# Optimization experiments

Hardware: AMD Instinct MI355X
Metric: run time of the kernel (lower is better)

## Reference

```python
import jax, jax.numpy as jnp
import numpy as np
from jax import lax

# Stacked SimpleRNN (Keras): h_t = tanh(x_t @ W + h_{t-1} @ U + b).
# Dropout(0.5) is only active in training mode; this reference implements
# inference (training=None -> dropout disabled), matching model(x).

B, T, F = 512, 512, 78
HIDDENS = (16, 32, 64, 70)
NUM_CLASSES = 5


def _glorot(key, shape):
    fan_in, fan_out = shape[0], shape[1]
    lim = float(np.sqrt(6.0 / (fan_in + fan_out)))
    return jax.random.uniform(key, shape, jnp.float32, -lim, lim)


def setup_inputs() -> dict:
    key = jax.random.key(0)
    ks = jax.random.split(key, 16)
    x = jax.random.normal(ks[0], (B, T, F), jnp.float32)
    params = {}
    in_dim = F
    for i, h in enumerate(HIDDENS):
        params[f"W{i}"] = _glorot(ks[1 + 3 * i], (in_dim, h))
        params[f"U{i}"] = _glorot(ks[2 + 3 * i], (h, h))
        params[f"b{i}"] = jnp.zeros((h,), jnp.float32)
        in_dim = h
    params["Wd"] = _glorot(ks[13], (HIDDENS[-1], NUM_CLASSES))
    params["bd"] = jnp.zeros((NUM_CLASSES,), jnp.float32)
    return {"x": x, **params}


def _simple_rnn(x, W, U, b, return_sequences):
    # Precompute input projection for all timesteps: [B, T, H]
    xw = jnp.einsum("btf,fh->bth", x, W) + b
    h0 = jnp.zeros((x.shape[0], W.shape[1]), x.dtype)

    def step(h, xw_t):
        h_new = jnp.tanh(xw_t + h @ U)
        return h_new, h_new

    h_last, hs = lax.scan(step, h0, jnp.swapaxes(xw, 0, 1))  # scan over time
    if return_sequences:
        return jnp.swapaxes(hs, 0, 1)  # [B, T, H]
    return h_last  # [B, H]


def reference(x, W0, U0, b0, W1, U1, b1, W2, U2, b2, W3, U3, b3, Wd, bd):
    h = _simple_rnn(x, W0, U0, b0, True)
    h = _simple_rnn(h, W1, U1, b1, True)
    h = _simple_rnn(h, W2, U2, b2, True)
    h = _simple_rnn(h, W3, U3, b3, False)  # [B, 70]
    logits = h @ Wd + bd  # [B, 5]
    return jax.nn.softmax(logits, axis=-1)
```

## Files before the change

kernel.cpp:

```cpp
#include <hip/hip_runtime.h>
#include <cstddef>
#include <cstdint>


#define BB 512
#define TT 512
#define M_TOTAL (BB * TT)

__device__ __forceinline__ float tanh_fast(float x) {
  float ax = fabsf(x);
  float e = __expf(ax + ax);
  float r = 1.0f - 2.0f / (e + 1.0f);
  return (x >= 0.0f) ? r : -r;
}

__device__ __forceinline__ void fma4(float4& a, float s, const float4 w) {
  a.x = fmaf(s, w.x, a.x);
  a.y = fmaf(s, w.y, a.y);
  a.z = fmaf(s, w.z, a.z);
  a.w = fmaf(s, w.w, a.w);
}

template<int K, int N, int CG>
__global__ __launch_bounds__(256)
void proj_kernel(const float* __restrict__ in, const float* __restrict__ W,
                 const float* __restrict__ bias, float* __restrict__ out, int M)
{
  constexpr int NP = CG * 4;
  constexpr int RG = 256 / CG;
  __shared__ __align__(16) float wlds[K][NP];
  __shared__ __align__(16) float blds[NP];
  const int tid = threadIdx.x;
  for (int idx = tid; idx < K * NP; idx += 256) {
    int k = idx / NP, jj = idx - k * NP;
    wlds[k][jj] = (jj < N) ? W[k * N + jj] : 0.0f;
  }
  if (tid < NP) blds[tid] = (tid < N) ? bias[tid] : 0.0f;
  __syncthreads();

  const int c = tid % CG;
  const int rg = tid / CG;
  if (rg >= RG) return;
  const int j0 = c * 4;
  const long row0 = (long)blockIdx.x * (RG * 4) + (long)rg * 4;

  float4 b4 = *reinterpret_cast<const float4*>(&blds[j0]);
  float4 acc[4] = {b4, b4, b4, b4};
  const float* inp[4];
  bool rv[4];
  #pragma unroll
  for (int rr = 0; rr < 4; ++rr) {
    long rowi = row0 + rr;
    rv[rr] = rowi < M;
    inp[rr] = in + (rv[rr] ? rowi : 0) * (long)K;
  }

  int k = 0;
  for (; k + 4 <= K; k += 4) {
    float4 w0 = *reinterpret_cast<const float4*>(&wlds[k + 0][j0]);
    float4 w1 = *reinterpret_cast<const float4*>(&wlds[k + 1][j0]);
    float4 w2 = *reinterpret_cast<const float4*>(&wlds[k + 2][j0]);
    float4 w3 = *reinterpret_cast<const float4*>(&wlds[k + 3][j0]);
    #pragma unroll
    for (int rr = 0; rr < 4; ++rr) {
      float2 i0 = *reinterpret_cast<const float2*>(inp[rr] + k);
      float2 i1 = *reinterpret_cast<const float2*>(inp[rr] + k + 2);
      fma4(acc[rr], i0.x, w0);
      fma4(acc[rr], i0.y, w1);
      fma4(acc[rr], i1.x, w2);
      fma4(acc[rr], i1.y, w3);
    }
  }
  for (; k < K; ++k) {
    float4 w0 = *reinterpret_cast<const float4*>(&wlds[k][j0]);
    #pragma unroll
    for (int rr = 0; rr < 4; ++rr) fma4(acc[rr], inp[rr][k], w0);
  }

  #pragma unroll
  for (int rr = 0; rr < 4; ++rr) {
    if (!rv[rr]) continue;
    long obase = (row0 + rr) * (long)N + j0;
    if constexpr ((N % 4) == 0) {
      *reinterpret_cast<float4*>(&out[obase]) = acc[rr];
    } else {
      if (j0 + 4 <= N) {
        *reinterpret_cast<float2*>(&out[obase]) = make_float2(acc[rr].x, acc[rr].y);
        *reinterpret_cast<float2*>(&out[obase + 2]) = make_float2(acc[rr].z, acc[rr].w);
      } else {
        float v[4] = {acc[rr].x, acc[rr].y, acc[rr].z, acc[rr].w};
        #pragma unroll
        for (int jj = 0; jj < 4; ++jj)
          if (j0 + jj < N) out[obase + jj] = v[jj];
      }
    }
  }
}

template<int H, int ROWS, int BLK, bool LAST>
__global__ __launch_bounds__(BLK)
void rec_kernel(const float* __restrict__ xw, const float* __restrict__ U,
                float* __restrict__ hseq,
                const float* __restrict__ Wd, const float* __restrict__ bd,
                float* __restrict__ outp)
{
  constexpr int HP = (H + 3) & ~3;
  const int tid = threadIdx.x;
  const int r = tid / H;
  const int j = tid - r * H;
  const bool active = (r < ROWS);
  const int rc = active ? r : 0;
  int row = blockIdx.x * ROWS + r;
  if (row >= BB) row = BB - 1;

  __shared__ __align__(16) float hbuf[2][ROWS][HP];
  __shared__ float slog[8];
  for (int i = tid; i < 2 * ROWS * HP; i += BLK)
    reinterpret_cast<float*>(hbuf)[i] = 0.0f;

  float u[HP];
  #pragma unroll
  for (int kk = 0; kk < HP; ++kk)
    u[kk] = (kk < H && active) ? U[kk * H + j] : 0.0f;

  const float* xwrow = xw + ((size_t)row * TT) * H + j;
  float* hout = hseq + ((size_t)row * TT) * H + j;
  __syncthreads();

  float p0 = xwrow[0];
  float p1 = xwrow[H];
  for (int t = 0; t < TT; ++t) {
    float xv = p0;
    p0 = p1;
    int tn = (t + 2 < TT) ? (t + 2) : (TT - 1);
    p1 = xwrow[(size_t)tn * H];

    const float* hb = &hbuf[t & 1][rc][0];
    float a0 = xv, a1 = 0.0f, a2 = 0.0f, a3 = 0.0f;
    #pragma unroll
    for (int k4 = 0; k4 < HP / 4; ++k4) {
      float4 h4 = *reinterpret_cast<const float4*>(hb + 4 * k4);
      a0 = fmaf(h4.x, u[4 * k4 + 0], a0);
      a1 = fmaf(h4.y, u[4 * k4 + 1], a1);
      a2 = fmaf(h4.z, u[4 * k4 + 2], a2);
      a3 = fmaf(h4.w, u[4 * k4 + 3], a3);
    }
    float hn = tanh_fast((a0 + a1) + (a2 + a3));
    if (active) {
      hbuf[(t & 1) ^ 1][r][j] = hn;
      if constexpr (!LAST) hout[(size_t)t * H] = hn;
    }
    __syncthreads();
  }

  if constexpr (LAST) {
    if (tid < 5) {
      float l = bd[tid];
      #pragma unroll
      for (int kk = 0; kk < H; ++kk)
        l = fmaf(hbuf[0][0][kk], Wd[kk * 5 + tid], l);
      slog[tid] = l;
    }
    __syncthreads();
    if (tid < 5) {
      float m = slog[0];
      #pragma unroll
      for (int i = 1; i < 5; ++i) m = fmaxf(m, slog[i]);
      float s = 0.0f;
      #pragma unroll
      for (int i = 0; i < 5; ++i) s += __expf(slog[i] - m);
      outp[(size_t)blockIdx.x * 5 + tid] = __expf(slog[tid] - m) / s;
    }
  }
}

extern "C" void kernel_launch(void* const* d_in, const int* in_sizes, int n_in,
                              void* d_out, int out_size, void* d_ws, size_t ws_size,
                              hipStream_t stream)
{
  const float* x  = (const float*)d_in[0];
  const float* W0 = (const float*)d_in[1];
  const float* U0 = (const float*)d_in[2];
  const float* b0 = (const float*)d_in[3];
  const float* W1 = (const float*)d_in[4];
  const float* U1 = (const float*)d_in[5];
  const float* b1 = (const float*)d_in[6];
  const float* W2 = (const float*)d_in[7];
  const float* U2 = (const float*)d_in[8];
  const float* b2 = (const float*)d_in[9];
  const float* W3 = (const float*)d_in[10];
  const float* U3 = (const float*)d_in[11];
  const float* b3 = (const float*)d_in[12];
  const float* Wd = (const float*)d_in[13];
  const float* bd = (const float*)d_in[14];
  float* outp = (float*)d_out;

  float* A  = (float*)d_ws;
  float* Bv = (float*)((char*)d_ws + 73400320);

  const int M = M_TOTAL;

  proj_kernel<78, 16, 4><<<M / 256, 256, 0, stream>>>(x, W0, b0, A, M);
  rec_kernel<16, 4, 64, false><<<BB / 4, 64, 0, stream>>>(A, U0, Bv, Wd, bd, outp);
  proj_kernel<16, 32, 8><<<M / 128, 256, 0, stream>>>(Bv, W1, b1, A, M);
  rec_kernel<32, 2, 64, false><<<BB / 2, 64, 0, stream>>>(A, U1, Bv, Wd, bd, outp);
  proj_kernel<32, 64, 16><<<M / 64, 256, 0, stream>>>(Bv, W2, b2, A, M);
  rec_kernel<64, 1, 64, false><<<BB, 64, 0, stream>>>(A, U2, Bv, Wd, bd, outp);
  proj_kernel<64, 70, 18><<<(M + 55) / 56, 256, 0, stream>>>(Bv, W3, b3, A, M);
  rec_kernel<70, 1, 128, true><<<BB, 128, 0, stream>>>(A, U3, Bv, Wd, bd, outp);
}
```

Before: 1.129 ms.

## Run recurrence in a single wavefront without barriers and deeper prefetch

Every recurrent layer now runs in one 64-thread wavefront per block. The __syncthreads and double-buffered hidden state are replaced by a single LDS buffer, relying on lockstep wavefront execution. The H=70 layer gets its own kernel where the first six lanes compute two outputs each, so the block shrinks from 128 threads to one wave. The xw prefetch depth grows from 2 to 8 steps, and the final softmax uses wave shuffles. This removes per-step barrier cost but depends on implicit wave-synchronous LDS ordering, which may be fragile; register pressure also rises.

```diff
diff --git a/kernel.cpp b/kernel.cpp
--- a/kernel.cpp
+++ b/kernel.cpp
@@ -97,81 +97,136 @@
   }
 }
 
-template<int H, int ROWS, int BLK, bool LAST>
-__global__ __launch_bounds__(BLK)
+template<int H, int ROWS>
+__global__ __launch_bounds__(64, 1)
 void rec_kernel(const float* __restrict__ xw, const float* __restrict__ U,
-                float* __restrict__ hseq,
-                const float* __restrict__ Wd, const float* __restrict__ bd,
-                float* __restrict__ outp)
+                float* __restrict__ hseq)
 {
   constexpr int HP = (H + 3) & ~3;
+  constexpr int PF = 8;
   const int tid = threadIdx.x;
   const int r = tid / H;
   const int j = tid - r * H;
-  const bool active = (r < ROWS);
-  const int rc = active ? r : 0;
-  int row = blockIdx.x * ROWS + r;
-  if (row >= BB) row = BB - 1;
-
-  __shared__ __align__(16) float hbuf[2][ROWS][HP];
-  __shared__ float slog[8];
-  for (int i = tid; i < 2 * ROWS * HP; i += BLK)
-    reinterpret_cast<float*>(hbuf)[i] = 0.0f;
+  const int row = blockIdx.x * ROWS + r;
+
+  __shared__ __align__(16) float hlds[ROWS][HP];
+  for (int i = tid; i < ROWS * HP; i += 64)
+    reinterpret_cast<float*>(hlds)[i] = 0.0f;
+  __syncthreads();
 
   float u[HP];
   #pragma unroll
-  for (int kk = 0; kk < HP; ++kk)
-    u[kk] = (kk < H && active) ? U[kk * H + j] : 0.0f;
+  for (int kk = 0; kk < HP; ++kk) {
+    u[kk] = (kk < H) ? U[kk * H + j] : 0.0f;
+    asm volatile("" : "+v"(u[kk]));
+  }
 
   const float* xwrow = xw + ((size_t)row * TT) * H + j;
   float* hout = hseq + ((size_t)row * TT) * H + j;
+
+  float pf[PF];
+  #pragma unroll
+  for (int d = 0; d < PF; ++d) pf[d] = xwrow[(size_t)d * H];
+
+  for (int t = 0; t < TT; t += PF) {
+    #pragma unroll
+    for (int d = 0; d < PF; ++d) {
+      float xv = pf[d];
+      int tn = t + d + PF;
+      tn = (tn < TT) ? tn : (TT - 1);
+      pf[d] = xwrow[(size_t)tn * H];
+
+      const float* hb = &hlds[r][0];
+      float a0 = xv, a1 = 0.0f, a2 = 0.0f, a3 = 0.0f;
+      #pragma unroll
+      for (int k4 = 0; k4 < HP / 4; ++k4) {
+        float4 h4 = *reinterpret_cast<const float4*>(hb + 4 * k4);
+        a0 = fmaf(h4.x, u[4 * k4 + 0], a0);
+        a1 = fmaf(h4.y, u[4 * k4 + 1], a1);
+        a2 = fmaf(h4.z, u[4 * k4 + 2], a2);
+        a3 = fmaf(h4.w, u[4 * k4 + 3], a3);
+      }
+      float hn = tanh_fast((a0 + a1) + (a2 + a3));
+      hlds[r][j] = hn;
+      hout[(size_t)(t + d) * H] = hn;
+    }
+  }
+}
+
+__global__ __launch_bounds__(64, 1)
+void rec70_kernel(const float* __restrict__ xw, const float* __restrict__ U,
+                  const float* __restrict__ Wd, const float* __restrict__ bd,
+                  float* __restrict__ outp)
+{
+  constexpr int H = 70, HP = 72, PF = 8;
+  const int tid = threadIdx.x;
+  const int row = blockIdx.x;
+  const int j2 = (tid < 6) ? (64 + tid) : 69;
+
+  __shared__ __align__(16) float hlds[HP];
+  for (int i = tid; i < HP; i += 64) hlds[i] = 0.0f;
   __syncthreads();
 
-  float p0 = xwrow[0];
-  float p1 = xwrow[H];
-  for (int t = 0; t < TT; ++t) {
-    float xv = p0;
-    p0 = p1;
-    int tn = (t + 2 < TT) ? (t + 2) : (TT - 1);
-    p1 = xwrow[(size_t)tn * H];
-
-    const float* hb = &hbuf[t & 1][rc][0];
-    float a0 = xv, a1 = 0.0f, a2 = 0.0f, a3 = 0.0f;
-    #pragma unroll
-    for (int k4 = 0; k4 < HP / 4; ++k4) {
-      float4 h4 = *reinterpret_cast<const float4*>(hb + 4 * k4);
-      a0 = fmaf(h4.x, u[4 * k4 + 0], a0);
-      a1 = fmaf(h4.y, u[4 * k4 + 1], a1);
-      a2 = fmaf(h4.z, u[4 * k4 + 2], a2);
-      a3 = fmaf(h4.w, u[4 * k4 + 3], a3);
-    }
-    float hn = tanh_fast((a0 + a1) + (a2 + a3));
-    if (active) {
-      hbuf[(t & 1) ^ 1][r][j] = hn;
-      if constexpr (!LAST) hout[(size_t)t * H] = hn;
-    }
-    __syncthreads();
-  }
-
-  if constexpr (LAST) {
-    if (tid < 5) {
-      float l = bd[tid];
+  float u[HP], u2[HP];
+  #pragma unroll
+  for (int kk = 0; kk < HP; ++kk) {
+    u[kk]  = (kk < H) ? U[kk * H + tid] : 0.0f;
+    u2[kk] = (kk < H && tid < 6) ? U[kk * H + 64 + tid] : 0.0f;
+    asm volatile("" : "+v"(u[kk]), "+v"(u2[kk]));
+  }
+
+  const float* xwrow = xw + ((size_t)row * TT) * H;
+  float pfA[PF], pfB[PF];
+  #pragma unroll
+  for (int d = 0; d < PF; ++d) {
+    pfA[d] = xwrow[(size_t)d * H + tid];
+    pfB[d] = xwrow[(size_t)d * H + j2];
+  }
+
+  for (int t = 0; t < TT; t += PF) {
+    #pragma unroll
+    for (int d = 0; d < PF; ++d) {
+      float xvA = pfA[d], xvB = pfB[d];
+      int tn = t + d + PF;
+      tn = (tn < TT) ? tn : (TT - 1);
+      pfA[d] = xwrow[(size_t)tn * H + tid];
+      pfB[d] = xwrow[(size_t)tn * H + j2];
+
+      float a0 = xvA, a1 = 0.0f, a2 = 0.0f, a3 = 0.0f;
+      float b0 = xvB, b1 = 0.0f, b2 = 0.0f, b3 = 0.0f;
       #pragma unroll
-      for (int kk = 0; kk < H; ++kk)
-        l = fmaf(hbuf[0][0][kk], Wd[kk * 5 + tid], l);
-      slog[tid] = l;
-    }
-    __syncthreads();
-    if (tid < 5) {
-      float m = slog[0];
-      #pragma unroll
-      for (int i = 1; i < 5; ++i) m = fmaxf(m, slog[i]);
-      float s = 0.0f;
-      #pragma unroll
-      for (int i = 0; i < 5; ++i) s += __expf(slog[i] - m);
-      outp[(size_t)blockIdx.x * 5 + tid] = __expf(slog[tid] - m) / s;
-    }
-  }
+      for (int k4 = 0; k4 < HP / 4; ++k4) {
+        float4 h4 = *reinterpret_cast<const float4*>(&hlds[4 * k4]);
+        a0 = fmaf(h4.x, u[4 * k4 + 0], a0);
+        a1 = fmaf(h4.y, u[4 * k4 + 1], a1);
+        a2 = fmaf(h4.z, u[4 * k4 + 2], a2);
+        a3 = fmaf(h4.w, u[4 * k4 + 3], a3);
+        b0 = fmaf(h4.x, u2[4 * k4 + 0], b0);
+        b1 = fmaf(h4.y, u2[4 * k4 + 1], b1);
+        b2 = fmaf(h4.z, u2[4 * k4 + 2], b2);
+        b3 = fmaf(h4.w, u2[4 * k4 + 3], b3);
+      }
+      float hnA = tanh_fast((a0 + a1) + (a2 + a3));
+      float hnB = tanh_fast((b0 + b1) + (b2 + b3));
+      hlds[tid] = hnA;
+      if (tid < 6) hlds[64 + tid] = hnB;
+    }
+  }
+
+  float l = 0.0f;
+  if (tid < 5) {
+    l = bd[tid];
+    #pragma unroll
+    for (int kk = 0; kk < H; ++kk)
+      l = fmaf(hlds[kk], Wd[kk * 5 + tid], l);
+  }
+  float l0 = __shfl(l, 0), l1 = __shfl(l, 1), l2 = __shfl(l, 2),
+        l3 = __shfl(l, 3), l4 = __shfl(l, 4);
+  float m = fmaxf(fmaxf(fmaxf(l0, l1), fmaxf(l2, l3)), l4);
+  float s = __expf(l0 - m) + __expf(l1 - m) + __expf(l2 - m) +
+            __expf(l3 - m) + __expf(l4 - m);
+  if (tid < 5)
+    outp[(size_t)row * 5 + tid] = __expf(l - m) / s;
 }
 
 extern "C" void kernel_launch(void* const* d_in, const int* in_sizes, int n_in,
@@ -201,11 +256,11 @@
   const int M = M_TOTAL;
 
   proj_kernel<78, 16, 4><<<M / 256, 256, 0, stream>>>(x, W0, b0, A, M);
-  rec_kernel<16, 4, 64, false><<<BB / 4, 64, 0, stream>>>(A, U0, Bv, Wd, bd, outp);
+  rec_kernel<16, 4><<<BB / 4, 64, 0, stream>>>(A, U0, Bv);
   proj_kernel<16, 32, 8><<<M / 128, 256, 0, stream>>>(Bv, W1, b1, A, M);
-  rec_kernel<32, 2, 64, false><<<BB / 2, 64, 0, stream>>>(A, U1, Bv, Wd, bd, outp);
+  rec_kernel<32, 2><<<BB / 2, 64, 0, stream>>>(A, U1, Bv);
   proj_kernel<32, 64, 16><<<M / 64, 256, 0, stream>>>(Bv, W2, b2, A, M);
-  rec_kernel<64, 1, 64, false><<<BB, 64, 0, stream>>>(A, U2, Bv, Wd, bd, outp);
+  rec_kernel<64, 1><<<BB, 64, 0, stream>>>(A, U2, Bv);
   proj_kernel<64, 70, 18><<<(M + 55) / 56, 256, 0, stream>>>(Bv, W3, b3, A, M);
-  rec_kernel<70, 1, 128, true><<<BB, 128, 0, stream>>>(A, U3, Bv, Wd, bd, outp);
-}
+  rec70_kernel<<<BB, 64, 0, stream>>>(A, U3, Wd, bd, outp);
+}
```

New measurement: 962.2 us. 1.17x faster.
